# Kernel optimization log

Measured on AMD Instinct MI355X. Metric: run time of the kernel, lower is better.

Reference implementation:

```python
import jax, jax.numpy as jnp
import numpy as np

B, C, N = 4, 256, 2048
H = 8
HD = C // H  # head_dim = 32


def setup_inputs() -> dict:
    key = jax.random.key(0)
    ks = jax.random.split(key, 5)
    s = 1.0 / np.sqrt(C)
    return {
        "x": jax.random.normal(ks[0], (B, C, 3, N), dtype=jnp.float32),
        "Wq": jax.random.normal(ks[1], (C, C), dtype=jnp.float32) * s,
        "Wk": jax.random.normal(ks[2], (C, C), dtype=jnp.float32) * s,
        "Wv": jax.random.normal(ks[3], (C, C), dtype=jnp.float32) * s,
        "Wo": jax.random.normal(ks[4], (C, C), dtype=jnp.float32) * s,
    }


def _vn_linear(W, x):
    # nn.Linear over channel axis: out[b,o,d,n] = sum_c W[o,c] x[b,c,d,n]
    return jnp.einsum('oc,bcdn->bodn', W, x)


def _heads(t):
    # [B,C,3,N] -> [B,H,N,HD,3]
    return t.reshape(B, H, HD, 3, N).transpose(0, 1, 4, 2, 3)


def reference(x, Wq, Wk, Wv, Wo):
    q = _heads(_vn_linear(Wq, x))
    k = _heads(_vn_linear(Wk, x))
    v = _heads(_vn_linear(Wv, x))
    # energy contracts over (head_dim, 3)
    energy = jnp.einsum('bhnci,bhmci->bhnm', q, k)
    attn = jax.nn.softmax(energy / np.sqrt(HD), axis=-1)
    out = jnp.einsum('bhnm,bhmci->bhnci', attn, v)
    # [B,H,N,HD,3] -> [B,C,3,N]
    out = out.transpose(0, 1, 3, 4, 2).reshape(B, C, 3, N)
    out = _vn_linear(Wo, out)
    return out + x
```

## Files before the change

### kernel.cpp

```cpp
#include <hip/hip_runtime.h>
#include <hip/hip_bf16.h>
#include <cmath>


typedef unsigned short u16;
typedef unsigned int   u32;
typedef u16   u16x8  __attribute__((ext_vector_type(8)));
typedef short s16x8  __attribute__((ext_vector_type(8)));
typedef float f32x4  __attribute__((ext_vector_type(4)));
typedef float f32x16 __attribute__((ext_vector_type(16)));

namespace {
constexpr int Nc = 2048, Fc = 96;
constexpr float SCALE_LOG2 = 0.17677669529663687f * 1.4426950408889634f;
constexpr int KP = 104;
constexpr int VP = 40;
constexpr int VOFF = 32 * KP;
constexpr int SBUF = VOFF + 96 * VP;
}

__device__ inline float fast_exp2(float x) {
#if __has_builtin(__builtin_amdgcn_exp2f)
    return __builtin_amdgcn_exp2f(x);
#else
    return exp2f(x);
#endif
}

__device__ inline u16 f2bf(float x) {
    union { float f; unsigned u; } v; v.f = x;
    unsigned r = v.u + 0x7FFFu + ((v.u >> 16) & 1u);
    return (u16)(r >> 16);
}

__device__ inline float bf2f(u16 x) {
    union { unsigned u; float f; } v; v.u = ((unsigned)x) << 16; return v.f;
}

__global__ __launch_bounds__(256) void wconv_kernel(
    const float* __restrict__ Wq, const float* __restrict__ Wk,
    const float* __restrict__ Wv, const float* __restrict__ Wo,
    u16* __restrict__ Wb)
{
    const int id = blockIdx.x * 256 + threadIdx.x;
    const int base = id * 8;
    const int o = base >> 8, c = base & 255;
    const int sel = o >> 8, ol = o & 255;
    const float* src = (sel == 0) ? Wq : (sel == 1) ? Wk : (sel == 2) ? Wv : Wo;
    const float sc = (sel == 0) ? SCALE_LOG2 : 1.0f;
    const float4 a = *(const float4*)&src[(size_t)ol * 256 + c];
    const float4 b = *(const float4*)&src[(size_t)ol * 256 + c + 4];
    u16x8 r;
    r[0]=f2bf(a.x*sc); r[1]=f2bf(a.y*sc); r[2]=f2bf(a.z*sc); r[3]=f2bf(a.w*sc);
    r[4]=f2bf(b.x*sc); r[5]=f2bf(b.y*sc); r[6]=f2bf(b.z*sc); r[7]=f2bf(b.w*sc);
    *(u16x8*)&Wb[(size_t)o * 256 + c] = r;
}

__global__ __launch_bounds__(256) void xt_kernel(
    const float* __restrict__ x, u16* __restrict__ xt)
{
    const int nt = blockIdx.x, ct = blockIdx.y, bi = blockIdx.z;
    const int b = bi / 3, i = bi % 3;
    const int t = (int)threadIdx.x;
    const int n0 = nt * 64, c0 = ct * 64;

    __shared__ u16 tile[64][72];

    const int n_l = t & 63;
#pragma unroll
    for (int it = 0; it < 16; ++it) {
        const int c_l = (t >> 6) + it * 4;
        tile[n_l][c_l] =
            f2bf(x[(((size_t)(b * 256 + c0 + c_l)) * 3 + i) * Nc + n0 + n_l]);
    }
    __syncthreads();
#pragma unroll
    for (int it = 0; it < 2; ++it) {
        const int idx = t + it * 256;
        const int nn = idx >> 3, part = idx & 7;
        *(u16x8*)&xt[((size_t)bi * Nc + n0 + nn) * 256 + c0 + part * 8] =
            *(const u16x8*)&tile[nn][part * 8];
    }
}

__global__ __launch_bounds__(256) void qkv_gemm_kernel(
    const u16* __restrict__ xt, const u16* __restrict__ wb,
    u16* __restrict__ Qt, u16* __restrict__ Kt, u16* __restrict__ Vf)
{
    const int nt = blockIdx.x;
    const int wy = blockIdx.y;
    const int bi = blockIdx.z;
    const int b = bi / 3, i = bi % 3;
    const int wsel = wy >> 1, ot = wy & 1;

    const u16* xs = xt + ((size_t)bi * Nc + nt * 128) * 256;
    const u16* ws = wb + (size_t)(wsel * 256 + ot * 128) * 256;

    __shared__ u16 xl[128][40];
    __shared__ u16 wl[128][40];

    const int t = (int)threadIdx.x;
    const int wv = t >> 6, lane = t & 63;
    const int g = lane >> 4, c16 = lane & 15;
    const int wr = wv >> 1, wc = wv & 1;

    f32x4 acc[4][4];
#pragma unroll
    for (int mi = 0; mi < 4; ++mi)
#pragma unroll
        for (int ni = 0; ni < 4; ++ni)
#pragma unroll
            for (int r = 0; r < 4; ++r) acc[mi][ni][r] = 0.f;

    for (int ks = 0; ks < 8; ++ks) {
        __syncthreads();
#pragma unroll
        for (int it = 0; it < 2; ++it) {
            const int idx = t + it * 256;
            const int row = idx >> 2, part = idx & 3;
            *(u16x8*)&xl[row][part * 8] =
                *(const u16x8*)&xs[(size_t)row * 256 + ks * 32 + part * 8];
            *(u16x8*)&wl[row][part * 8] =
                *(const u16x8*)&ws[(size_t)row * 256 + ks * 32 + part * 8];
        }
        __syncthreads();

        s16x8 af[4], bf[4];
        if (wsel < 2) {
#pragma unroll
            for (int mi = 0; mi < 4; ++mi) af[mi] = *(const s16x8*)&xl[wr*64 + mi*16 + c16][g*8];
#pragma unroll
            for (int ni = 0; ni < 4; ++ni) bf[ni] = *(const s16x8*)&wl[wc*64 + ni*16 + c16][g*8];
        } else {
#pragma unroll
            for (int mi = 0; mi < 4; ++mi) af[mi] = *(const s16x8*)&wl[wr*64 + mi*16 + c16][g*8];
#pragma unroll
            for (int ni = 0; ni < 4; ++ni) bf[ni] = *(const s16x8*)&xl[wc*64 + ni*16 + c16][g*8];
        }
#pragma unroll
        for (int mi = 0; mi < 4; ++mi)
#pragma unroll
            for (int ni = 0; ni < 4; ++ni)
                acc[mi][ni] = __builtin_amdgcn_mfma_f32_16x16x32_bf16(
                    af[mi], bf[ni], acc[mi][ni], 0, 0, 0);
    }

    if (wsel < 2) {
        u16* dst = wsel ? Kt : Qt;
#pragma unroll
        for (int mi = 0; mi < 4; ++mi)
#pragma unroll
            for (int ni = 0; ni < 4; ++ni) {
                const int o = ot * 128 + wc * 64 + ni * 16 + c16;
                const int h = o >> 5, cw = o & 31;
#pragma unroll
                for (int r = 0; r < 4; ++r) {
                    const int n = nt * 128 + wr * 64 + mi * 16 + g * 4 + r;
                    dst[((size_t)(b * 8 + h) * Nc + n) * Fc + i * 32 + cw] =
                        f2bf(acc[mi][ni][r]);
                }
            }
    } else {
#pragma unroll
        for (int mi = 0; mi < 4; ++mi)
#pragma unroll
            for (int ni = 0; ni < 4; ++ni) {
                const int n = nt * 128 + wc * 64 + ni * 16 + c16;
#pragma unroll
                for (int r = 0; r < 4; ++r) {
                    const int o = ot * 128 + wr * 64 + mi * 16 + g * 4 + r;
                    const int h = o >> 5, cw = o & 31;
                    Vf[((size_t)(b * 8 + h) * Fc + i * 32 + cw) * Nc + n] =
                        f2bf(acc[mi][ni][r]);
                }
            }
    }
}

__global__ __launch_bounds__(256) void attn_mfma_kernel(
    const u16* __restrict__ Qt, const u16* __restrict__ Kt,
    const u16* __restrict__ Vf, u16* __restrict__ obt, float* __restrict__ lP)
{
    const int bid = (int)blockIdx.x;
    const int lid = (bid & 7) * 128 + (bid >> 3);
    const int bh   = lid >> 5;
    const int r5   = lid & 31;
    const int qt   = r5 >> 1;
    const int half = r5 & 1;

    const int t_   = (int)threadIdx.x;
    const int wq   = t_ >> 6;
    const int lane = t_ & 63;
    const int ql   = lane & 31;
    const int hi   = lane >> 5;

    __shared__ u16 sbuf[3 * SBUF];

    const int qb = qt * 128 + wq * 32;
    const int k0 = half * 1024;

    s16x8 bq[6];
#pragma unroll
    for (int s6 = 0; s6 < 6; ++s6)
        bq[s6] = *(const s16x8*)&Qt[((size_t)bh * Nc + qb + ql) * Fc + s6 * 16 + hi * 8];

    const u16* g_cur[3]; int g_str[3], g_dst[3];
#pragma unroll
    for (int it = 0; it < 3; ++it) {
        const int c = t_ + it * 256;
        if (c < 384) {
            const int row = c / 12, part = c - row * 12;
            g_cur[it] = Kt + ((size_t)bh * Nc + k0 + row) * Fc + part * 8;
            g_str[it] = 32 * Fc;
            g_dst[it] = row * KP + part * 8;
        } else {
            const int c2 = c - 384, f = c2 >> 2, part = c2 & 3;
            g_cur[it] = Vf + ((size_t)bh * Fc + f) * Nc + k0 + part * 8;
            g_str[it] = 32;
            g_dst[it] = VOFF + f * VP + part * 8;
        }
    }

    f32x16 acc[3];
#pragma unroll
    for (int ft = 0; ft < 3; ++ft)
#pragma unroll
        for (int r = 0; r < 16; ++r) acc[ft][r] = 0.f;
    float lacc[8];
#pragma unroll
    for (int r = 0; r < 8; ++r) lacc[r] = 0.f;

    u16* b0 = sbuf;
    u16* b1 = sbuf + SBUF;
    u16* b2 = sbuf + 2 * SBUF;

    u16x8 sreg[3];
#pragma unroll
    for (int it = 0; it < 3; ++it) { sreg[it] = *(const u16x8*)g_cur[it]; g_cur[it] += g_str[it]; }
#pragma unroll
    for (int it = 0; it < 3; ++it) *(u16x8*)&b0[g_dst[it]] = sreg[it];
#pragma unroll
    for (int it = 0; it < 3; ++it) { sreg[it] = *(const u16x8*)g_cur[it]; g_cur[it] += g_str[it]; }
    __syncthreads();

    f32x16 svE, svO;
#pragma unroll
    for (int r = 0; r < 16; ++r) svE[r] = 0.f;
#pragma unroll
    for (int s6 = 0; s6 < 6; ++s6) {
        const s16x8 ka = *(const s16x8*)&b0[ql * KP + s6 * 16 + hi * 8];
        svE = __builtin_amdgcn_mfma_f32_32x32x16_bf16(ka, bq[s6], svE, 0, 0, 0);
    }
#pragma unroll
    for (int it = 0; it < 3; ++it) *(u16x8*)&b1[g_dst[it]] = sreg[it];
#pragma unroll
    for (int it = 0; it < 3; ++it) { sreg[it] = *(const u16x8*)g_cur[it]; g_cur[it] += g_str[it]; }
    __syncthreads();

    u16 *bA = b0, *bB = b1, *bC = b2;

    auto body = [&](int t, f32x16& SC, f32x16& SN) {
        if (t < 31) {
#pragma unroll
            for (int r = 0; r < 16; ++r) SN[r] = 0.f;
#pragma unroll
            for (int s6 = 0; s6 < 6; ++s6) {
                const s16x8 ka = *(const s16x8*)&bB[ql * KP + s6 * 16 + hi * 8];
                SN = __builtin_amdgcn_mfma_f32_32x32x16_bf16(ka, bq[s6], SN, 0, 0, 0);
            }
        }
        if (t < 30) {
#pragma unroll
            for (int it = 0; it < 3; ++it) *(u16x8*)&bC[g_dst[it]] = sreg[it];
        }
        if (t < 29) {
#pragma unroll
            for (int it = 0; it < 3; ++it) { sreg[it] = *(const u16x8*)g_cur[it]; g_cur[it] += g_str[it]; }
        }

#pragma unroll
        for (int r = 0; r < 16; ++r) SC[r] = fast_exp2(SC[r]);
#pragma unroll
        for (int r = 0; r < 8; ++r) lacc[r] += SC[r] + SC[r + 8];

        u32 pk8[8];
#pragma unroll
        for (int j = 0; j < 8; ++j)
            asm("v_cvt_pk_bf16_f32 %0, %1, %2" : "=v"(pk8[j]) : "v"(SC[2*j]), "v"(SC[2*j+1]));
        asm volatile("v_permlane32_swap_b32 %0, %1" : "+v"(pk8[0]), "+v"(pk8[2]));
        asm volatile("v_permlane32_swap_b32 %0, %1" : "+v"(pk8[1]), "+v"(pk8[3]));
        asm volatile("v_permlane32_swap_b32 %0, %1" : "+v"(pk8[4]), "+v"(pk8[6]));
        asm volatile("v_permlane32_swap_b32 %0, %1" : "+v"(pk8[5]), "+v"(pk8[7]));
        union U { u32 w[4]; s16x8 v; } pb0, pb1;
        pb0.w[0]=pk8[0]; pb0.w[1]=pk8[1]; pb0.w[2]=pk8[2]; pb0.w[3]=pk8[3];
        pb1.w[0]=pk8[4]; pb1.w[1]=pk8[5]; pb1.w[2]=pk8[6]; pb1.w[3]=pk8[7];

#pragma unroll
        for (int ft = 0; ft < 3; ++ft) {
            const s16x8 va0 = *(const s16x8*)&bA[VOFF + (ft * 32 + ql) * VP + hi * 8];
            acc[ft] = __builtin_amdgcn_mfma_f32_32x32x16_bf16(va0, pb0.v, acc[ft], 0, 0, 0);
            const s16x8 va1 = *(const s16x8*)&bA[VOFF + (ft * 32 + ql) * VP + 16 + hi * 8];
            acc[ft] = __builtin_amdgcn_mfma_f32_32x32x16_bf16(va1, pb1.v, acc[ft], 0, 0, 0);
        }

        if (t < 31) __syncthreads();
    };

    for (int tb = 0; tb < 16; ++tb) {
        body(2 * tb, svE, svO);
        { u16* tmp = bA; bA = bB; bB = bC; bC = tmp; }
        body(2 * tb + 1, svO, svE);
        { u16* tmp = bA; bA = bB; bB = bC; bC = tmp; }
    }

    float l4[4];
#pragma unroll
    for (int r = 0; r < 4; ++r) l4[r] = lacc[r] + lacc[r + 4];
    float l_s = (l4[0] + l4[2]) + (l4[1] + l4[3]);
    l_s += __shfl_xor(l_s, 32);
    const float inv = 1.f / l_s;
    if (hi == 0)
        lP[((size_t)half * 32 + bh) * Nc + qb + ql] = l_s;

    __syncthreads();
    u16* ot = sbuf + wq * 3328;
#pragma unroll
    for (int ft = 0; ft < 3; ++ft)
#pragma unroll
        for (int r = 0; r < 16; ++r) {
            const int frow = (r & 3) + 8 * (r >> 2) + 4 * hi;
            ot[ql * 104 + ft * 32 + frow] = f2bf(acc[ft][r] * inv);
        }
    __syncthreads();

    u16x8 v6[6];
#pragma unroll
    for (int j = 0; j < 6; ++j)
        v6[j] = *(const u16x8*)&ot[ql * 104 + hi * 48 + j * 8];

    const int n = qb + ql;
    const int b_ = bh >> 3, h_ = bh & 7;
    const size_t base0 = (((size_t)half * 12 + b_ * 3 + 0) * Nc + n) * 256 + h_ * 32;
    const size_t base1 = (((size_t)half * 12 + b_ * 3 + 1) * Nc + n) * 256 + h_ * 32;
    const size_t base2 = (((size_t)half * 12 + b_ * 3 + 2) * Nc + n) * 256 + h_ * 32;
    if (hi == 0) {
        *(u16x8*)&obt[base0 +  0] = v6[0];
        *(u16x8*)&obt[base0 +  8] = v6[1];
        *(u16x8*)&obt[base0 + 16] = v6[2];
        *(u16x8*)&obt[base0 + 24] = v6[3];
        *(u16x8*)&obt[base1 +  0] = v6[4];
        *(u16x8*)&obt[base1 +  8] = v6[5];
    } else {
        *(u16x8*)&obt[base1 + 16] = v6[0];
        *(u16x8*)&obt[base1 + 24] = v6[1];
        *(u16x8*)&obt[base2 +  0] = v6[2];
        *(u16x8*)&obt[base2 +  8] = v6[3];
        *(u16x8*)&obt[base2 + 16] = v6[4];
        *(u16x8*)&obt[base2 + 24] = v6[5];
    }
}

__global__ __launch_bounds__(256) void out_gemm_kernel(
    const u16* __restrict__ obt, const float* __restrict__ lP,
    const u16* __restrict__ wb, const float* __restrict__ x,
    float* __restrict__ out)
{
    const int nt = blockIdx.x, ot = blockIdx.y, bi = blockIdx.z;
    const int b = bi / 3, i = bi % 3;

    const u16* p0 = obt + ((size_t)bi * Nc) * 256;
    const u16* p1 = obt + (((size_t)12 + bi) * Nc) * 256;
    const u16* ws = wb + (size_t)(768 + ot * 128) * 256;

    __shared__ u16 al[128][40];
    __shared__ u16 wl[128][40];

    const int t = (int)threadIdx.x;
    const int wv = t >> 6, lane = t & 63;
    const int g = lane >> 4, c16 = lane & 15;
    const int wr = wv >> 1, wc = wv & 1;

    f32x4 acc[4][4];
#pragma unroll
    for (int mi = 0; mi < 4; ++mi)
#pragma unroll
        for (int ni = 0; ni < 4; ++ni)
#pragma unroll
            for (int r = 0; r < 4; ++r) acc[mi][ni][r] = 0.f;

    for (int ks = 0; ks < 8; ++ks) {
        __syncthreads();
#pragma unroll
        for (int it = 0; it < 2; ++it) {
            const int idx = t + it * 256;
            const int row = idx >> 2, part = idx & 3;
            const int n = nt * 128 + row;
            const float l0 = lP[((size_t)(b * 8 + ks)) * Nc + n];
            const float l1 = lP[((size_t)(32 + b * 8 + ks)) * Nc + n];
            const float w0 = l0 / (l0 + l1);
            const float w1 = 1.f - w0;
            const u16x8 a0 = *(const u16x8*)&p0[(size_t)n * 256 + ks * 32 + part * 8];
            const u16x8 a1 = *(const u16x8*)&p1[(size_t)n * 256 + ks * 32 + part * 8];
            u16x8 rr;
#pragma unroll
            for (int j = 0; j < 8; ++j)
                rr[j] = f2bf(bf2f(a0[j]) * w0 + bf2f(a1[j]) * w1);
            *(u16x8*)&al[row][part * 8] = rr;
            *(u16x8*)&wl[row][part * 8] =
                *(const u16x8*)&ws[(size_t)row * 256 + ks * 32 + part * 8];
        }
        __syncthreads();

        s16x8 af[4], bf[4];
#pragma unroll
        for (int mi = 0; mi < 4; ++mi) af[mi] = *(const s16x8*)&wl[wr*64 + mi*16 + c16][g*8];
#pragma unroll
        for (int ni = 0; ni < 4; ++ni) bf[ni] = *(const s16x8*)&al[wc*64 + ni*16 + c16][g*8];
#pragma unroll
        for (int mi = 0; mi < 4; ++mi)
#pragma unroll
            for (int ni = 0; ni < 4; ++ni)
                acc[mi][ni] = __builtin_amdgcn_mfma_f32_16x16x32_bf16(
                    af[mi], bf[ni], acc[mi][ni], 0, 0, 0);
    }

#pragma unroll
    for (int mi = 0; mi < 4; ++mi)
#pragma unroll
        for (int ni = 0; ni < 4; ++ni) {
            const int n = nt * 128 + wc * 64 + ni * 16 + c16;
#pragma unroll
            for (int r = 0; r < 4; ++r) {
                const int o = ot * 128 + wr * 64 + mi * 16 + g * 4 + r;
                const size_t idx = ((size_t)(b * 256 + o) * 3 + i) * Nc + n;
                out[idx] = x[idx] + acc[mi][ni][r];
            }
        }
}

extern "C" void kernel_launch(void* const* d_in, const int* in_sizes, int n_in,
                              void* d_out, int out_size, void* d_ws, size_t ws_size,
                              hipStream_t stream) {
    const float* x  = (const float*)d_in[0];
    const float* Wq = (const float*)d_in[1];
    const float* Wk = (const float*)d_in[2];
    const float* Wv = (const float*)d_in[3];
    const float* Wo = (const float*)d_in[4];
    float* out = (float*)d_out;

    const size_t E = (size_t)32 * Fc * Nc;
    u16* xt  = (u16*)d_ws;
    u16* wbw = xt + E;
    u16* qt  = wbw + 262144;
    u16* kt  = qt + E;
    u16* vf  = kt + E;
    u16* obt = vf + E;
    float* lP = (float*)(obt + 2 * E);

    dim3 blk(256);
    wconv_kernel    <<<dim3(128),        blk, 0, stream>>>(Wq, Wk, Wv, Wo, wbw);
    xt_kernel       <<<dim3(32, 4, 12),  blk, 0, stream>>>(x, xt);
    qkv_gemm_kernel <<<dim3(16, 6, 12),  blk, 0, stream>>>(xt, wbw, qt, kt, vf);
    attn_mfma_kernel<<<dim3(1024),       blk, 0, stream>>>(qt, kt, vf, obt, lP);
    out_gemm_kernel <<<dim3(16, 2, 12),  blk, 0, stream>>>(obt, lP, wbw, x, out);
}
```

Measured before the change: 120.6 us.

## Load K/V fragments directly from global memory, dropping shared-memory triple buffering

Replaces the cooperative shared-memory triple-buffered K/V staging and its per-tile barriers with per-wave direct global loads of K and V MFMA fragments into registers. Each wave now reads its own operands (relying on L2/L1 for reuse across the four waves), and the epilogue transpose uses a per-wave LDS region with only a waitcnt instead of block barriers. This removes LDS traffic and __syncthreads stalls but loses the software pipelining of loads against compute and multiplies global load traffic by the wave count, so latency may be exposed.

```diff
diff --git a/kernel.cpp b/kernel.cpp
--- a/kernel.cpp
+++ b/kernel.cpp
@@ -13,10 +13,6 @@
 namespace {
 constexpr int Nc = 2048, Fc = 96;
 constexpr float SCALE_LOG2 = 0.17677669529663687f * 1.4426950408889634f;
-constexpr int KP = 104;
-constexpr int VP = 40;
-constexpr int VOFF = 32 * KP;
-constexpr int SBUF = VOFF + 96 * VP;
 }
 
 __device__ inline float fast_exp2(float x) {
@@ -194,7 +190,7 @@
     const int ql   = lane & 31;
     const int hi   = lane >> 5;
 
-    __shared__ u16 sbuf[3 * SBUF];
+    __shared__ u16 tbuf[4][3328];
 
     const int qb = qt * 128 + wq * 32;
     const int k0 = half * 1024;
@@ -204,22 +200,10 @@
     for (int s6 = 0; s6 < 6; ++s6)
         bq[s6] = *(const s16x8*)&Qt[((size_t)bh * Nc + qb + ql) * Fc + s6 * 16 + hi * 8];
 
-    const u16* g_cur[3]; int g_str[3], g_dst[3];
-#pragma unroll
-    for (int it = 0; it < 3; ++it) {
-        const int c = t_ + it * 256;
-        if (c < 384) {
-            const int row = c / 12, part = c - row * 12;
-            g_cur[it] = Kt + ((size_t)bh * Nc + k0 + row) * Fc + part * 8;
-            g_str[it] = 32 * Fc;
-            g_dst[it] = row * KP + part * 8;
-        } else {
-            const int c2 = c - 384, f = c2 >> 2, part = c2 & 3;
-            g_cur[it] = Vf + ((size_t)bh * Fc + f) * Nc + k0 + part * 8;
-            g_str[it] = 32;
-            g_dst[it] = VOFF + f * VP + part * 8;
-        }
-    }
+    const u16* kp  = Kt + ((size_t)bh * Nc + k0 + ql) * Fc + hi * 8;
+    const u16* vp0 = Vf + ((size_t)bh * Fc +  0 + ql) * Nc + k0 + hi * 8;
+    const u16* vp1 = Vf + ((size_t)bh * Fc + 32 + ql) * Nc + k0 + hi * 8;
+    const u16* vp2 = Vf + ((size_t)bh * Fc + 64 + ql) * Nc + k0 + hi * 8;
 
     f32x16 acc[3];
 #pragma unroll
@@ -230,63 +214,32 @@
 #pragma unroll
     for (int r = 0; r < 8; ++r) lacc[r] = 0.f;
 
-    u16* b0 = sbuf;
-    u16* b1 = sbuf + SBUF;
-    u16* b2 = sbuf + 2 * SBUF;
-
-    u16x8 sreg[3];
-#pragma unroll
-    for (int it = 0; it < 3; ++it) { sreg[it] = *(const u16x8*)g_cur[it]; g_cur[it] += g_str[it]; }
-#pragma unroll
-    for (int it = 0; it < 3; ++it) *(u16x8*)&b0[g_dst[it]] = sreg[it];
-#pragma unroll
-    for (int it = 0; it < 3; ++it) { sreg[it] = *(const u16x8*)g_cur[it]; g_cur[it] += g_str[it]; }
-    __syncthreads();
-
-    f32x16 svE, svO;
-#pragma unroll
-    for (int r = 0; r < 16; ++r) svE[r] = 0.f;
-#pragma unroll
-    for (int s6 = 0; s6 < 6; ++s6) {
-        const s16x8 ka = *(const s16x8*)&b0[ql * KP + s6 * 16 + hi * 8];
-        svE = __builtin_amdgcn_mfma_f32_32x32x16_bf16(ka, bq[s6], svE, 0, 0, 0);
-    }
-#pragma unroll
-    for (int it = 0; it < 3; ++it) *(u16x8*)&b1[g_dst[it]] = sreg[it];
-#pragma unroll
-    for (int it = 0; it < 3; ++it) { sreg[it] = *(const u16x8*)g_cur[it]; g_cur[it] += g_str[it]; }
-    __syncthreads();
-
-    u16 *bA = b0, *bB = b1, *bC = b2;
-
-    auto body = [&](int t, f32x16& SC, f32x16& SN) {
-        if (t < 31) {
-#pragma unroll
-            for (int r = 0; r < 16; ++r) SN[r] = 0.f;
-#pragma unroll
-            for (int s6 = 0; s6 < 6; ++s6) {
-                const s16x8 ka = *(const s16x8*)&bB[ql * KP + s6 * 16 + hi * 8];
-                SN = __builtin_amdgcn_mfma_f32_32x32x16_bf16(ka, bq[s6], SN, 0, 0, 0);
-            }
-        }
-        if (t < 30) {
-#pragma unroll
-            for (int it = 0; it < 3; ++it) *(u16x8*)&bC[g_dst[it]] = sreg[it];
-        }
-        if (t < 29) {
-#pragma unroll
-            for (int it = 0; it < 3; ++it) { sreg[it] = *(const u16x8*)g_cur[it]; g_cur[it] += g_str[it]; }
-        }
-
-#pragma unroll
-        for (int r = 0; r < 16; ++r) SC[r] = fast_exp2(SC[r]);
-#pragma unroll
-        for (int r = 0; r < 8; ++r) lacc[r] += SC[r] + SC[r + 8];
+    for (int kt = 0; kt < 32; ++kt) {
+        s16x8 ka[6], va[6];
+#pragma unroll
+        for (int s6 = 0; s6 < 6; ++s6)
+            ka[s6] = *(const s16x8*)(kp + s6 * 16);
+        va[0] = *(const s16x8*)(vp0);      va[1] = *(const s16x8*)(vp0 + 16);
+        va[2] = *(const s16x8*)(vp1);      va[3] = *(const s16x8*)(vp1 + 16);
+        va[4] = *(const s16x8*)(vp2);      va[5] = *(const s16x8*)(vp2 + 16);
+        kp += 32 * Fc; vp0 += 32; vp1 += 32; vp2 += 32;
+
+        f32x16 sv;
+#pragma unroll
+        for (int r = 0; r < 16; ++r) sv[r] = 0.f;
+#pragma unroll
+        for (int s6 = 0; s6 < 6; ++s6)
+            sv = __builtin_amdgcn_mfma_f32_32x32x16_bf16(ka[s6], bq[s6], sv, 0, 0, 0);
+
+#pragma unroll
+        for (int r = 0; r < 16; ++r) sv[r] = fast_exp2(sv[r]);
+#pragma unroll
+        for (int r = 0; r < 8; ++r) lacc[r] += sv[r] + sv[r + 8];
 
         u32 pk8[8];
 #pragma unroll
         for (int j = 0; j < 8; ++j)
-            asm("v_cvt_pk_bf16_f32 %0, %1, %2" : "=v"(pk8[j]) : "v"(SC[2*j]), "v"(SC[2*j+1]));
+            asm("v_cvt_pk_bf16_f32 %0, %1, %2" : "=v"(pk8[j]) : "v"(sv[2*j]), "v"(sv[2*j+1]));
         asm volatile("v_permlane32_swap_b32 %0, %1" : "+v"(pk8[0]), "+v"(pk8[2]));
         asm volatile("v_permlane32_swap_b32 %0, %1" : "+v"(pk8[1]), "+v"(pk8[3]));
         asm volatile("v_permlane32_swap_b32 %0, %1" : "+v"(pk8[4]), "+v"(pk8[6]));
@@ -297,20 +250,9 @@
 
 #pragma unroll
         for (int ft = 0; ft < 3; ++ft) {
-            const s16x8 va0 = *(const s16x8*)&bA[VOFF + (ft * 32 + ql) * VP + hi * 8];
-            acc[ft] = __builtin_amdgcn_mfma_f32_32x32x16_bf16(va0, pb0.v, acc[ft], 0, 0, 0);
-            const s16x8 va1 = *(const s16x8*)&bA[VOFF + (ft * 32 + ql) * VP + 16 + hi * 8];
-            acc[ft] = __builtin_amdgcn_mfma_f32_32x32x16_bf16(va1, pb1.v, acc[ft], 0, 0, 0);
-        }
-
-        if (t < 31) __syncthreads();
-    };
-
-    for (int tb = 0; tb < 16; ++tb) {
-        body(2 * tb, svE, svO);
-        { u16* tmp = bA; bA = bB; bB = bC; bC = tmp; }
-        body(2 * tb + 1, svO, svE);
-        { u16* tmp = bA; bA = bB; bB = bC; bC = tmp; }
+            acc[ft] = __builtin_amdgcn_mfma_f32_32x32x16_bf16(va[2*ft],     pb0.v, acc[ft], 0, 0, 0);
+            acc[ft] = __builtin_amdgcn_mfma_f32_32x32x16_bf16(va[2*ft + 1], pb1.v, acc[ft], 0, 0, 0);
+        }
     }
 
     float l4[4];
@@ -322,8 +264,7 @@
     if (hi == 0)
         lP[((size_t)half * 32 + bh) * Nc + qb + ql] = l_s;
 
-    __syncthreads();
-    u16* ot = sbuf + wq * 3328;
+    u16* ot = &tbuf[wq][0];
 #pragma unroll
     for (int ft = 0; ft < 3; ++ft)
 #pragma unroll
@@ -331,7 +272,8 @@
             const int frow = (r & 3) + 8 * (r >> 2) + 4 * hi;
             ot[ql * 104 + ft * 32 + frow] = f2bf(acc[ft][r] * inv);
         }
-    __syncthreads();
+    asm volatile("s_waitcnt lgkmcnt(0)" ::: "memory");
+    __builtin_amdgcn_sched_barrier(0);
 
     u16x8 v6[6];
 #pragma unroll
```

After: 192.1 us. 1.59x slower.
